# Kernel optimization log

Measured on AMD Instinct MI355X. Metric: run time of the kernel, lower is better.

The kernel has to match this reference:

```python
import jax, jax.numpy as jnp
import numpy as np

V = 100000
E = 1600000
IN_CH = 128
HEADS = 4
OUT_CH = 16
NEG_SLOPE = 0.2


def setup_inputs() -> dict:
    key = jax.random.key(0)
    k1, k2, k3, k4, k5 = jax.random.split(key, 5)
    x = jax.random.normal(k1, (V, IN_CH), dtype=jnp.float32)
    edge_index = jax.random.randint(k2, (2, E), 0, V, dtype=jnp.int32)
    # Xavier-ish scaled params
    W = jax.random.normal(k3, (IN_CH, HEADS * OUT_CH), dtype=jnp.float32) / np.sqrt(IN_CH)
    a_src = jax.random.normal(k4, (HEADS, OUT_CH), dtype=jnp.float32) / np.sqrt(OUT_CH)
    a_dst = jax.random.normal(k5, (HEADS, OUT_CH), dtype=jnp.float32) / np.sqrt(OUT_CH)
    return {"x": x, "edge_index": edge_index, "W": W, "a_src": a_src, "a_dst": a_dst}


def reference(x, edge_index, W, a_src, a_dst):
    v = x.shape[0]
    h, cout = a_src.shape
    z = (x @ W).reshape(v, h, cout)                      # [V,H,C]
    src, dst = edge_index[0], edge_index[1]
    # per-node attention logits, then gather at edges (same math as gather-then-dot)
    e_src = jnp.einsum("vhc,hc->vh", z, a_src)           # [V,H]
    e_dst = jnp.einsum("vhc,hc->vh", z, a_dst)           # [V,H]
    e = jax.nn.leaky_relu(e_src[src] + e_dst[dst], NEG_SLOPE)  # [E,H]
    # scatter softmax over dst per head
    m = jax.ops.segment_max(e, dst, num_segments=v)      # [V,H]
    # nodes with no incoming edges get -inf max; edges never reference them
    exp_e = jnp.exp(e - m[dst])                          # [E,H]
    denom = jax.ops.segment_sum(exp_e, dst, num_segments=v)  # [V,H]
    alpha = exp_e / (denom[dst] + 1e-9)                  # [E,H]
    # scatter aggregation of weighted source features
    agg = jax.ops.segment_sum(z[src] * alpha[:, :, None], dst, num_segments=v)  # [V,H,C]
    out = jax.nn.elu(agg)
    return out.reshape(v, h * cout)
```

## Files before the change

kernel.cpp:

```cpp
#include <hip/hip_runtime.h>
#include <hip/hip_bf16.h>
#include <cstdint>

#define NV 100000
#define NE 1600000
#define KIN 128
#define NH 4
#define NC 16
#define NF 64
#define NBKT 1563
#define BCAP 1216
#define EPW 16
#define BINWG 196
#define GEMMWG 782
#define NITEMS 978
#define XSTR 136

typedef __attribute__((ext_vector_type(8))) short bf16x8;
typedef __attribute__((ext_vector_type(4))) float f32x4;

__device__ __forceinline__ short f2bf(float f) {
    unsigned u = __float_as_uint(f);
    return (short)((u + 0x7FFFu + ((u >> 16) & 1u)) >> 16);
}

__device__ __forceinline__ unsigned enc11(float w) {
    unsigned t = (__float_as_uint(w) + 0x10000u) >> 17;
    t = min(max(t, 7168u), 9215u);
    return t - 7168u;
}

__device__ __forceinline__ float declo(unsigned u) {
    return __uint_as_float(u << 16);
}
__device__ __forceinline__ float dechi(unsigned u) {
    return __uint_as_float(u & 0xFFFF0000u);
}

__global__ __launch_bounds__(512) void k_front(
    const float* __restrict__ x, const float* __restrict__ W,
    const float* __restrict__ a_src, const float* __restrict__ a_dst,
    __hip_bfloat16* __restrict__ z, float* __restrict__ esrc,
    float* __restrict__ edst,
    const int* __restrict__ ei, int* __restrict__ gcur,
    unsigned* __restrict__ barr)
{
    __shared__ union SM {
        struct { int hist[NBKT]; int base[NBKT]; } bin;
        short xs[128 * XSTR];
    } sm;

    const int bi = blockIdx.x;
    const int t = threadIdx.x;

    if (bi % 5 == 0) {
        int* hist = sm.bin.hist;
        int* base = sm.bin.base;
        const int e0 = (bi / 5) * (512 * EPW);

        for (int i = t; i < NBKT; i += 512) hist[i] = 0;
        __syncthreads();

        unsigned pk[EPW];
        short bk[EPW];
#pragma unroll
        for (int i = 0; i < EPW; ++i) {
            const int e = e0 + i * 512 + t;
            if (e < NE) {
                const int s = ei[e];
                const int d = ei[NE + e];
                const int bkt = d >> 6;
                bk[i] = (short)bkt;
                pk[i] = ((unsigned)(d & 63) << 17) | (unsigned)s;
                atomicAdd(&hist[bkt], 1);
            } else {
                bk[i] = -1;
            }
        }
        __syncthreads();
        for (int i = t; i < NBKT; i += 512) {
            const int c = hist[i];
            base[i] = c ? atomicAdd(&gcur[i], c) : 0;
            hist[i] = 0;
        }
        __syncthreads();
#pragma unroll
        for (int i = 0; i < EPW; ++i) {
            if (bk[i] >= 0) {
                const int bkt = bk[i];
                const int pos = base[bkt] + atomicAdd(&hist[bkt], 1);
                if (pos < BCAP)
                    barr[(size_t)bkt * BCAP + pos] = pk[i];
            }
        }
    } else {
        short* xs = sm.xs;
        const int id = bi - bi / 5 - 1;
        const float4* __restrict__ x4 = (const float4*)x;

#pragma unroll
        for (int i = 0; i < 8; ++i) {
            const int li = i * 512 + t;
            const int idx = id * 4096 + li;
            float4 v = make_float4(0.f, 0.f, 0.f, 0.f);
            if (idx < NV * (KIN / 4)) v = x4[idx];
            const unsigned lo = (unsigned)(unsigned short)f2bf(v.x)
                              | ((unsigned)(unsigned short)f2bf(v.y) << 16);
            const unsigned hi = (unsigned)(unsigned short)f2bf(v.z)
                              | ((unsigned)(unsigned short)f2bf(v.w) << 16);
            *(uint2*)&xs[(li >> 5) * XSTR + (li & 31) * 4] = make_uint2(lo, hi);
        }
        __syncthreads();

        const int wv = t >> 6;
        const int lane = t & 63;
        const int n = lane & 15;
        const int quad = lane >> 4;

        bf16x8 bf[16];
#pragma unroll
        for (int ct = 0; ct < 4; ++ct) {
#pragma unroll
            for (int ks = 0; ks < 4; ++ks) {
                bf16x8 f;
#pragma unroll
                for (int j = 0; j < 8; ++j) {
                    const int k = ks * 32 + quad * 8 + j;
                    f[j] = f2bf(W[k * NF + ct * 16 + n]);
                }
                bf[ct * 4 + ks] = f;
            }
        }

        const short* __restrict__ arow = &xs[(wv * 16 + n) * XSTR];
        f32x4 acc[4];
#pragma unroll
        for (int ct = 0; ct < 4; ++ct) acc[ct] = (f32x4){0.f, 0.f, 0.f, 0.f};

#pragma unroll
        for (int ks = 0; ks < 4; ++ks) {
            const bf16x8 af = *(const bf16x8*)(arow + ks * 32 + quad * 8);
#pragma unroll
            for (int ct = 0; ct < 4; ++ct)
                acc[ct] = __builtin_amdgcn_mfma_f32_16x16x32_bf16(
                    af, bf[ct * 4 + ks], acc[ct], 0, 0, 0);
        }

        float as[4], ad[4];
#pragma unroll
        for (int ct = 0; ct < 4; ++ct) {
            as[ct] = a_src[ct * 16 + n];
            ad[ct] = a_dst[ct * 16 + n];
        }
        unsigned short* __restrict__ zz = (unsigned short*)z;
#pragma unroll
        for (int ct = 0; ct < 4; ++ct) {
#pragma unroll
            for (int reg = 0; reg < 4; ++reg) {
                const int r_g = id * 128 + wv * 16 + quad * 4 + reg;
                const float v = acc[ct][reg];
                float ps = v * as[ct];
                float pd = v * ad[ct];
#pragma unroll
                for (int m = 8; m >= 1; m >>= 1) {
                    ps += __shfl_xor(ps, m, 16);
                    pd += __shfl_xor(pd, m, 16);
                }
                if (r_g < NV) {
                    zz[(size_t)r_g * NF + ct * 16 + n] = (unsigned short)f2bf(v);
                    if (n == 0) {
                        esrc[r_g * NH + ct] = ps;
                        edst[r_g * NH + ct] = pd;
                    }
                }
            }
        }
    }
}

__global__ __launch_bounds__(256) void k_back(
    const int* __restrict__ gcur, const unsigned* __restrict__ barr,
    const float* __restrict__ esrc, const float* __restrict__ edst,
    const __hip_bfloat16* __restrict__ z, float* __restrict__ out)
{
    __shared__ __align__(16) unsigned arr[BCAP];
    __shared__ unsigned long long rec[BCAP];
    __shared__ int hist[64], off[64], cur[64];
    __shared__ float4 led[64];
    const int t = threadIdx.x;
    const int b = blockIdx.x;
    int f = gcur[b]; if (f > BCAP) f = BCAP;
    const unsigned* __restrict__ bp = barr + (size_t)b * BCAP;

    if (t < 64) {
        hist[t] = 0;
        const int d = b * 64 + t;
        led[t] = (d < NV) ? *(const float4*)(edst + (size_t)d * 4)
                          : make_float4(0.f, 0.f, 0.f, 0.f);
    }
    __syncthreads();
    const int f4 = f >> 2;
    for (int i = t; i < f4; i += 256) {
        const uint4 v = ((const uint4*)bp)[i];
        ((uint4*)arr)[i] = v;
        atomicAdd(&hist[v.x >> 17], 1);
        atomicAdd(&hist[v.y >> 17], 1);
        atomicAdd(&hist[v.z >> 17], 1);
        atomicAdd(&hist[v.w >> 17], 1);
    }
    for (int i = (f4 << 2) + t; i < f; i += 256) {
        const unsigned v = bp[i];
        arr[i] = v;
        atomicAdd(&hist[v >> 17], 1);
    }
    __syncthreads();
    if (t < 64) {
        const int h0 = hist[t];
        int s = h0;
#pragma unroll
        for (int m = 1; m < 64; m <<= 1) {
            const int u = __shfl_up(s, m, 64);
            if (t >= m) s += u;
        }
        off[t] = s - h0;
        cur[t] = 0;
    }
    __syncthreads();

    for (int i = t; i < f; i += 256) {
        const unsigned p = arr[i];
        const int dl = p >> 17;
        const unsigned s = p & 0x1FFFFu;
        const int slot = off[dl] + atomicAdd(&cur[dl], 1);
        const float4 e4 = *(const float4*)(esrc + (size_t)s * 4);
        const float4 ed = led[dl];
        float ev;
        ev = e4.x + ed.x; ev = ev > 0.f ? ev : 0.2f * ev;
        const unsigned w0 = enc11(__expf(ev));
        ev = e4.y + ed.y; ev = ev > 0.f ? ev : 0.2f * ev;
        const unsigned w1 = enc11(__expf(ev));
        ev = e4.z + ed.z; ev = ev > 0.f ? ev : 0.2f * ev;
        const unsigned w2 = enc11(__expf(ev));
        ev = e4.w + ed.w; ev = ev > 0.f ? ev : 0.2f * ev;
        const unsigned w3 = enc11(__expf(ev));
        rec[slot] = (unsigned long long)s
            | ((unsigned long long)w0 << 17)
            | ((unsigned long long)w1 << 28)
            | ((unsigned long long)w2 << 39)
            | ((unsigned long long)w3 << 50);
    }
    __syncthreads();

    const int wv = t >> 6;
    const int lane = t & 63;
    const int dstq = lane >> 4;
    const int li = lane & 15;
    const int sh = 17 + 11 * (li >> 2);
    const unsigned short* __restrict__ zb = (const unsigned short*)z + li * 4;

    for (int k = 0; k < 4; ++k) {
        const int dl = wv * 16 + k * 4 + dstq;
        const int d = b * 64 + dl;
        const int begin = off[dl];
        const int nd = hist[dl];
        float a0 = 0.f, a1 = 0.f, a2 = 0.f, a3 = 0.f, den = 0.f;
        for (int j = 0; j < nd; j += 2) {
            const unsigned long long r0 = rec[begin + j];
            const unsigned long long r1 =
                (j + 1 < nd) ? rec[begin + j + 1] : 0ull;
            const unsigned s0 = (unsigned)r0 & 0x1FFFFu;
            const unsigned s1 = (unsigned)r1 & 0x1FFFFu;
            const float w0 = __uint_as_float(
                ((((unsigned)(r0 >> sh)) & 0x7FFu) + 7168u) << 17);
            const float w1 = __uint_as_float(
                ((((unsigned)(r1 >> sh)) & 0x7FFu) + 7168u) << 17);
            const uint2 zv0 = *(const uint2*)(zb + ((size_t)s0 << 6));
            const uint2 zv1 = *(const uint2*)(zb + ((size_t)s1 << 6));
            a0 = fmaf(w0, declo(zv0.x), a0);
            a1 = fmaf(w0, dechi(zv0.x), a1);
            a2 = fmaf(w0, declo(zv0.y), a2);
            a3 = fmaf(w0, dechi(zv0.y), a3);
            a0 = fmaf(w1, declo(zv1.x), a0);
            a1 = fmaf(w1, dechi(zv1.x), a1);
            a2 = fmaf(w1, declo(zv1.y), a2);
            a3 = fmaf(w1, dechi(zv1.y), a3);
            den += w0 + w1;
        }
        if (d < NV) {
            const float id = 1.f / (den + 1e-9f);
            float v0 = a0 * id, v1 = a1 * id, v2 = a2 * id, v3 = a3 * id;
            v0 = v0 > 0.f ? v0 : __expf(v0) - 1.f;
            v1 = v1 > 0.f ? v1 : __expf(v1) - 1.f;
            v2 = v2 > 0.f ? v2 : __expf(v2) - 1.f;
            v3 = v3 > 0.f ? v3 : __expf(v3) - 1.f;
            *(float4*)(out + (size_t)d * NF + li * 4) =
                make_float4(v0, v1, v2, v3);
        }
    }
}

extern "C" void kernel_launch(void* const* d_in, const int* in_sizes, int n_in,
                              void* d_out, int out_size, void* d_ws, size_t ws_size,
                              hipStream_t stream)
{
    const float* x     = (const float*)d_in[0];
    const int*   ei    = (const int*)d_in[1];
    const float* W     = (const float*)d_in[2];
    const float* a_src = (const float*)d_in[3];
    const float* a_dst = (const float*)d_in[4];
    float* out = (float*)d_out;

    char* p = (char*)d_ws;
    __hip_bfloat16* z = (__hip_bfloat16*)p;  p += (size_t)NV * NF * 2;
    float* esrc = (float*)p;                 p += (size_t)NV * NH * 4;
    float* edst = (float*)p;                 p += (size_t)NV * NH * 4;
    int*   gcur = (int*)p;                   p += (size_t)NBKT * 4;
    p = (char*)(((uintptr_t)p + 255) & ~(uintptr_t)255);
    unsigned* barr = (unsigned*)p;           p += (size_t)NBKT * BCAP * 4;

    hipMemsetAsync(gcur, 0, (size_t)NBKT * 4, stream);
    k_front<<<NITEMS, 512, 0, stream>>>(x, W, a_src, a_dst, z, esrc, edst,
                                        ei, gcur, barr);
    k_back<<<NBKT, 256, 0, stream>>>(gcur, barr, esrc, edst, z, out);
}
```

Measured before the change: 174.4 us.

## Fold attention vectors into weight matrix and compute logits via extra MFMA tile

Precomputes W·a_src and W·a_dst per block into shared memory (128x8), converts them to bf16 and appends them as a fifth MFMA column tile, so the per-node attention logits come straight out of the GEMM. This replaces the per-element multiply and 4-step cross-lane shuffle reduction over 16 lanes for each of 16 outputs. The cost is an extra MFMA per k-step, more registers, a small per-block fp32 dot-product prologue and extra shared memory. Logits are now computed from bf16-rounded folded weights rather than from fp32 products of z, which slightly changes their precision.

```diff
diff --git a/kernel.cpp b/kernel.cpp
--- a/kernel.cpp
+++ b/kernel.cpp
@@ -47,7 +47,7 @@
 {
     __shared__ union SM {
         struct { int hist[NBKT]; int base[NBKT]; } bin;
-        short xs[128 * XSTR];
+        struct { short xs[128 * XSTR]; float wa[128 * 8]; } g;
     } sm;
 
     const int bi = blockIdx.x;
@@ -94,7 +94,8 @@
             }
         }
     } else {
-        short* xs = sm.xs;
+        short* xs = sm.g.xs;
+        float* wa = sm.g.wa;
         const int id = bi - bi / 5 - 1;
         const float4* __restrict__ x4 = (const float4*)x;
 
@@ -110,6 +111,19 @@
                               | ((unsigned)(unsigned short)f2bf(v.w) << 16);
             *(uint2*)&xs[(li >> 5) * XSTR + (li & 31) * 4] = make_uint2(lo, hi);
         }
+#pragma unroll
+        for (int i = t; i < 1024; i += 512) {
+            const int k = i >> 3;
+            const int h8 = i & 7;
+            const int h = h8 & 3;
+            const float* __restrict__ a =
+                (h8 < 4) ? (a_src + h * 16) : (a_dst + h * 16);
+            const float* __restrict__ wr = W + k * NF + h * 16;
+            float sum = 0.f;
+#pragma unroll
+            for (int c = 0; c < 16; ++c) sum += wr[c] * a[c];
+            wa[i] = sum;
+        }
         __syncthreads();
 
         const int wv = t >> 6;
@@ -117,7 +131,7 @@
         const int n = lane & 15;
         const int quad = lane >> 4;
 
-        bf16x8 bf[16];
+        bf16x8 bf[20];
 #pragma unroll
         for (int ct = 0; ct < 4; ++ct) {
 #pragma unroll
@@ -131,48 +145,49 @@
                 bf[ct * 4 + ks] = f;
             }
         }
+#pragma unroll
+        for (int ks = 0; ks < 4; ++ks) {
+            bf16x8 f;
+#pragma unroll
+            for (int j = 0; j < 8; ++j) {
+                const int k = ks * 32 + quad * 8 + j;
+                f[j] = (n < 8) ? f2bf(wa[k * 8 + n]) : (short)0;
+            }
+            bf[16 + ks] = f;
+        }
 
         const short* __restrict__ arow = &xs[(wv * 16 + n) * XSTR];
-        f32x4 acc[4];
-#pragma unroll
-        for (int ct = 0; ct < 4; ++ct) acc[ct] = (f32x4){0.f, 0.f, 0.f, 0.f};
+        f32x4 acc[5];
+#pragma unroll
+        for (int ct = 0; ct < 5; ++ct) acc[ct] = (f32x4){0.f, 0.f, 0.f, 0.f};
 
 #pragma unroll
         for (int ks = 0; ks < 4; ++ks) {
             const bf16x8 af = *(const bf16x8*)(arow + ks * 32 + quad * 8);
 #pragma unroll
-            for (int ct = 0; ct < 4; ++ct)
+            for (int ct = 0; ct < 5; ++ct)
                 acc[ct] = __builtin_amdgcn_mfma_f32_16x16x32_bf16(
                     af, bf[ct * 4 + ks], acc[ct], 0, 0, 0);
         }
 
-        float as[4], ad[4];
-#pragma unroll
-        for (int ct = 0; ct < 4; ++ct) {
-            as[ct] = a_src[ct * 16 + n];
-            ad[ct] = a_dst[ct * 16 + n];
-        }
         unsigned short* __restrict__ zz = (unsigned short*)z;
 #pragma unroll
         for (int ct = 0; ct < 4; ++ct) {
 #pragma unroll
             for (int reg = 0; reg < 4; ++reg) {
                 const int r_g = id * 128 + wv * 16 + quad * 4 + reg;
-                const float v = acc[ct][reg];
-                float ps = v * as[ct];
-                float pd = v * ad[ct];
-#pragma unroll
-                for (int m = 8; m >= 1; m >>= 1) {
-                    ps += __shfl_xor(ps, m, 16);
-                    pd += __shfl_xor(pd, m, 16);
-                }
-                if (r_g < NV) {
-                    zz[(size_t)r_g * NF + ct * 16 + n] = (unsigned short)f2bf(v);
-                    if (n == 0) {
-                        esrc[r_g * NH + ct] = ps;
-                        edst[r_g * NH + ct] = pd;
-                    }
-                }
+                if (r_g < NV)
+                    zz[(size_t)r_g * NF + ct * 16 + n] =
+                        (unsigned short)f2bf(acc[ct][reg]);
+            }
+        }
+#pragma unroll
+        for (int reg = 0; reg < 4; ++reg) {
+            const int r_g = id * 128 + wv * 16 + quad * 4 + reg;
+            if (r_g < NV && n < 8) {
+                const float v = acc[4][reg];
+                if (n < 4) esrc[r_g * NH + n] = v;
+                else       edst[r_g * NH + (n - 4)] = v;
             }
         }
     }
```

After: 192.2 us. 1.1x slower.
